# Kernel tuning notes

Hardware: AMD Instinct MI355X
Metric: run time of the kernel (lower is better)

## Reference

```python
import jax, jax.numpy as jnp
import numpy as np

C = 512
CR = C // 8  # reduced channels for b/c projections


def setup_inputs() -> dict:
    key = jax.random.key(0)
    ks = jax.random.split(key, 7)
    scale = 1.0 / np.sqrt(C)
    x = jax.random.normal(ks[0], (4, C, 64, 64), dtype=jnp.float32)
    Wb = jax.random.normal(ks[1], (CR, C), dtype=jnp.float32) * scale
    bb = jax.random.normal(ks[2], (CR,), dtype=jnp.float32) * 0.01
    Wc = jax.random.normal(ks[3], (CR, C), dtype=jnp.float32) * scale
    bc = jax.random.normal(ks[4], (CR,), dtype=jnp.float32) * 0.01
    Wd = jax.random.normal(ks[5], (C, C), dtype=jnp.float32) * scale
    bd = jax.random.normal(ks[6], (C,), dtype=jnp.float32) * 0.01
    return {"x": x, "Wb": Wb, "bb": bb, "Wc": Wc, "bc": bc, "Wd": Wd, "bd": bd}


def reference(x, Wb, bb, Wc, bc, Wd, bd):
    B, Cc, H, W = x.shape
    N = H * W
    xf = x.reshape(B, Cc, N)  # [B, C, N] (1x1 conv == per-position matmul)
    b = jnp.einsum('kc,bcn->bkn', Wb, xf) + bb[None, :, None]  # [B, CR, N]
    c = jnp.einsum('kc,bcn->bkn', Wc, xf) + bc[None, :, None]  # [B, CR, N]
    d = jnp.einsum('kc,bcn->bkn', Wd, xf) + bd[None, :, None]  # [B, C, N]
    # s[b,i,j] = sum_k b[b,k,i] * c[b,k,j]; softmax over j
    s = jnp.einsum('bki,bkj->bij', b, c)  # [B, N, N]
    s = jax.nn.softmax(s, axis=-1)
    # torch.bmm(d, s): y[b,c,j] = sum_i d[b,c,i] * s[b,i,j]
    y = jnp.einsum('bci,bij->bcj', d, s)  # [B, C, N]
    return x + y.reshape(B, Cc, H, W)
```

## Files before the change

### kernel.cpp

```cpp
#include <hip/hip_runtime.h>
#include <hip/hip_bf16.h>

typedef float f32x4 __attribute__((ext_vector_type(4)));
typedef float f32x16 __attribute__((ext_vector_type(16)));
typedef short s16x8 __attribute__((ext_vector_type(8)));
typedef uint  u32x4 __attribute__((ext_vector_type(4)));

#define MFMA_BF16(a, b, c) __builtin_amdgcn_mfma_f32_16x16x32_bf16((a), (b), (c), 0, 0, 0)
#define MFMA32(a, b, c)    __builtin_amdgcn_mfma_f32_32x32x16_bf16((a), (b), (c), 0, 0, 0)

__device__ __forceinline__ ushort f2bf(float f) {
  uint u = __builtin_bit_cast(uint, f);
  u += 0x7FFFu + ((u >> 16) & 1u);
  return (ushort)(u >> 16);
}
__device__ __forceinline__ uint pack2bf(float a, float b) {
  return (uint)f2bf(a) | ((uint)f2bf(b) << 16);
}
__device__ __forceinline__ float pexp(float s) {
  float t = fmaf(s, 1.4426950408889634f, -43.2808512266689f);
  float r;
  asm("v_exp_f32 %0, %1" : "=v"(r) : "v"(t));
  return r;
}
__device__ __forceinline__ uint cvtpk(float lo, float hi) {
  uint r;
  asm("v_cvt_pk_bf16_f32 %0, %1, %2" : "=v"(r) : "v"(lo), "v"(hi));
  return r;
}
__device__ __forceinline__ void plswap(uint& a, uint& b) {
  asm("v_permlane32_swap_b32 %0, %1" : "+v"(a), "+v"(b));
}
__device__ __forceinline__ void gld16(const void* g, void* l) {
  __builtin_amdgcn_global_load_lds(
      (const __attribute__((address_space(1))) unsigned int*)g,
      (__attribute__((address_space(3))) unsigned int*)l, 16, 0, 0);
}

#define WS_XT    0UL
#define WS_D     16777216UL
#define WS_BT    33554432UL
#define WS_CT    35651584UL
#define WS_WCAT  37748736UL
#define WS_BCAT  38404096UL

__global__ void k_prep_w(const float* __restrict__ Wb, const float* __restrict__ bb,
                         const float* __restrict__ Wc, const float* __restrict__ bc,
                         const float* __restrict__ Wd, const float* __restrict__ bd,
                         ushort* __restrict__ Wcat, float* __restrict__ bcat) {
  int idx = blockIdx.x * 256 + threadIdx.x;
  if (idx < 640 * 512) {
    int m = idx >> 9, k = idx & 511;
    float v = (m < 64) ? Wb[m * 512 + k] : (m < 128) ? Wc[(m - 64) * 512 + k] : Wd[(m - 128) * 512 + k];
    Wcat[idx] = f2bf(v);
  }
  if (idx < 640) {
    bcat[idx] = (idx < 64) ? bb[idx] : (idx < 128) ? bc[idx - 64] : bd[idx - 128];
  }
}

__global__ __launch_bounds__(256) void k_prep_xt(const float* __restrict__ x, ushort* __restrict__ xT) {
  __shared__ float tile[64][65];
  int bx = blockIdx.x;
  int b = bx >> 9;
  int c0 = ((bx >> 6) & 7) * 64;
  int n0 = (bx & 63) * 64;
  int t = threadIdx.x;
  const float* xb = x + (size_t)b * 512 * 4096;
#pragma unroll
  for (int p = 0; p < 4; ++p) {
    int cl = (t >> 4) + 16 * p;
    int nf = (t & 15) * 4;
    float4 v = *reinterpret_cast<const float4*>(xb + (size_t)(c0 + cl) * 4096 + n0 + nf);
    tile[cl][nf + 0] = v.x; tile[cl][nf + 1] = v.y; tile[cl][nf + 2] = v.z; tile[cl][nf + 3] = v.w;
  }
  __syncthreads();
  ushort* dst = xT + (size_t)b * 4096 * 512;
#pragma unroll
  for (int q = 0; q < 2; ++q) {
    int ch = t + 256 * q;
    int nl = ch >> 3;
    int cf = (ch & 7) * 8;
    uint4 o;
    o.x = pack2bf(tile[cf + 0][nl], tile[cf + 1][nl]);
    o.y = pack2bf(tile[cf + 2][nl], tile[cf + 3][nl]);
    o.z = pack2bf(tile[cf + 4][nl], tile[cf + 5][nl]);
    o.w = pack2bf(tile[cf + 6][nl], tile[cf + 7][nl]);
    *reinterpret_cast<uint4*>(dst + (size_t)(n0 + nl) * 512 + c0 + cf) = o;
  }
}

__global__ __launch_bounds__(256) void k_proj(const ushort* __restrict__ Wcat, const float* __restrict__ bcat,
                                              const ushort* __restrict__ xT, ushort* __restrict__ bT,
                                              ushort* __restrict__ cT, ushort* __restrict__ dmat) {
  int bx = blockIdx.x;
  int b = bx / 160;
  int r = bx % 160;
  int m0 = (r >> 5) * 128;
  int n0 = (r & 31) * 128;
  int t = threadIdx.x, l = t & 63, w = t >> 6;
  int wm = w >> 1, wn = w & 1, g = l >> 4, l15 = l & 15;
  const ushort* xb = xT + (size_t)b * 4096 * 512;
  f32x4 acc[4][4] = {};
  s16x8 bfn[4];
#pragma unroll
  for (int nt = 0; nt < 4; ++nt)
    bfn[nt] = *reinterpret_cast<const s16x8*>(xb + (size_t)(n0 + 64 * wn + 16 * nt + l15) * 512 + 8 * g);
  for (int k0 = 0; k0 < 512; k0 += 32) {
    s16x8 a[4], bf[4];
#pragma unroll
    for (int nt = 0; nt < 4; ++nt) bf[nt] = bfn[nt];
#pragma unroll
    for (int mt = 0; mt < 4; ++mt)
      a[mt] = *reinterpret_cast<const s16x8*>(Wcat + (size_t)(m0 + 64 * wm + 16 * mt + l15) * 512 + k0 + 8 * g);
    if (k0 + 32 < 512) {
#pragma unroll
      for (int nt = 0; nt < 4; ++nt)
        bfn[nt] = *reinterpret_cast<const s16x8*>(xb + (size_t)(n0 + 64 * wn + 16 * nt + l15) * 512 + k0 + 32 + 8 * g);
    }
    __builtin_amdgcn_sched_barrier(0);
#pragma unroll
    for (int mt = 0; mt < 4; ++mt)
#pragma unroll
      for (int nt = 0; nt < 4; ++nt)
        acc[mt][nt] = MFMA_BF16(a[mt], bf[nt], acc[mt][nt]);
  }
#pragma unroll
  for (int mt = 0; mt < 4; ++mt) {
    int mbase = m0 + 64 * wm + 16 * mt + 4 * g;
#pragma unroll
    for (int nt = 0; nt < 4; ++nt) {
      int n = n0 + 64 * wn + 16 * nt + l15;
      float vv[4];
      vv[0] = acc[mt][nt][0] + bcat[mbase + 0];
      vv[1] = acc[mt][nt][1] + bcat[mbase + 1];
      vv[2] = acc[mt][nt][2] + bcat[mbase + 2];
      vv[3] = acc[mt][nt][3] + bcat[mbase + 3];
      if (mbase < 64) {
        uint2 u2; u2.x = pack2bf(vv[0], vv[1]); u2.y = pack2bf(vv[2], vv[3]);
        size_t off = ((size_t)b * 4096 + n) * 64 + (size_t)((((mbase >> 3) ^ (n & 7)) << 3) + (mbase & 4));
        *reinterpret_cast<uint2*>(bT + off) = u2;
      } else if (mbase < 128) {
        uint2 u2; u2.x = pack2bf(vv[0], vv[1]); u2.y = pack2bf(vv[2], vv[3]);
        *reinterpret_cast<uint2*>(cT + ((size_t)b * 4096 + n) * 64 + (mbase - 64)) = u2;
      } else {
        int cc = mbase - 128;
        size_t fb = (((size_t)b * 256 + (n >> 4)) * 16) * 512;
#pragma unroll
        for (int rr = 0; rr < 4; ++rr) {
          int c = cc + rr;
          size_t idx = fb + (size_t)(c >> 5) * 512 + (size_t)(((n >> 3) & 1) * 32 + (c & 31)) * 8 + (n & 7);
          dmat[idx] = f2bf(vv[rr]);
        }
      }
    }
  }
}

__global__ __launch_bounds__(512) void k_stats(const ushort* __restrict__ bT, const ushort* __restrict__ cT,
                                               ushort* __restrict__ dmat) {
  __shared__ ushort sCT[3][8192];
  __shared__ float lsum[64];
  int bx = blockIdx.x;
  int b = bx >> 6;
  int i0 = (bx & 63) * 64;
  int t = threadIdx.x, l = t & 63, w = t >> 6;
  int wm = w >> 1, wn = w & 1, g = l >> 4, l15 = l & 15;
  if (t < 64) lsum[t] = 0.f;
  const ushort* bTb = bT + (size_t)b * 262144;
  const ushort* cTb = cT + (size_t)b * 262144;
  int arow = i0 + 16 * wm + l15;
  int r7 = arow & 7;
  const ushort* abase = bTb + (size_t)arow * 64;
  s16x8 a0 = *reinterpret_cast<const s16x8*>(abase + ((g ^ r7) << 3));
  s16x8 a1 = *reinterpret_cast<const s16x8*>(abase + (((g + 4) ^ r7) << 3));

  auto STAGE = [&](int jt) {
#pragma unroll
    for (int q = 0; q < 2; ++q) {
      int idx = t + 512 * q;
      int row = idx >> 3, u = idx & 7;
      gld16(cTb + (size_t)(jt * 128 + row) * 64 + ((u ^ (row & 7)) << 3),
            &sCT[jt % 3][idx * 8]);
    }
  };
  STAGE(0); STAGE(1);
  asm volatile("s_waitcnt vmcnt(2)" ::: "memory");
  __syncthreads();

  float lacc[4] = {0.f, 0.f, 0.f, 0.f};
  for (int jt = 0; jt < 32; ++jt) {
    if (jt + 2 < 32) STAGE(jt + 2);
    __builtin_amdgcn_sched_barrier(0);
    const ushort* cbuf = &sCT[jt % 3][0];
#pragma unroll
    for (int nt = 0; nt < 4; ++nt) {
      int row = 64 * wn + 16 * nt + l15;
      int rs = row & 7;
      s16x8 b0 = *reinterpret_cast<const s16x8*>(cbuf + row * 64 + ((g ^ rs) << 3));
      s16x8 b1 = *reinterpret_cast<const s16x8*>(cbuf + row * 64 + (((g + 4) ^ rs) << 3));
      f32x4 s = {0.f, 0.f, 0.f, 0.f};
      s = MFMA_BF16(a0, b0, s);
      s = MFMA_BF16(a1, b1, s);
#pragma unroll
      for (int rr = 0; rr < 4; ++rr) lacc[rr] += pexp(s[rr]);
    }
    if (jt < 30) { asm volatile("s_waitcnt vmcnt(2)" ::: "memory"); }
    else         { asm volatile("s_waitcnt vmcnt(0)" ::: "memory"); }
    __builtin_amdgcn_s_barrier();
  }
#pragma unroll
  for (int off = 1; off < 16; off <<= 1)
#pragma unroll
    for (int rr = 0; rr < 4; ++rr) lacc[rr] += __shfl_xor(lacc[rr], off);
  if (l15 == 0) {
#pragma unroll
    for (int rr = 0; rr < 4; ++rr) atomicAdd(&lsum[16 * wm + 4 * g + rr], lacc[rr]);
  }
  __syncthreads();
  if (t < 64) lsum[t] = 1.0f / fmaxf(lsum[t], 1e-30f);
  __syncthreads();
  int c = t;
  size_t rowb = (size_t)(c >> 5) * 512 + (size_t)(c & 31) * 8;
#pragma unroll
  for (int q = 0; q < 8; ++q) {
    int ic = (i0 >> 4) + (q >> 1);
    size_t idx = (((size_t)b * 256 + ic) * 16) * 512 + rowb + (size_t)(q & 1) * 256;
    s16x8 v = *reinterpret_cast<s16x8*>(dmat + idx);
    s16x8 nv;
#pragma unroll
    for (int e = 0; e < 8; ++e) {
      float f = __builtin_bit_cast(float, ((uint)(ushort)v[e]) << 16) * lsum[q * 8 + e];
      nv[e] = (short)f2bf(f);
    }
    *reinterpret_cast<s16x8*>(dmat + idx) = nv;
  }
}

__global__ __launch_bounds__(512, 2) void k_attn(const ushort* __restrict__ bT, const ushort* __restrict__ cT,
                                                 const ushort* __restrict__ dmat,
                                                 const float* __restrict__ x, float* __restrict__ out) {
  __shared__ ushort sBT[3][4096];
  __shared__ ushort sP[2][8192];
  int bid = blockIdx.x;
  int gid = (bid & 7) * 64 + (bid >> 3);
  int b   = gid >> 7;
  int cb  = (gid >> 5) & 3;
  int jB  = gid & 31;
  int t = threadIdx.x, w = t >> 6, l = t & 63;
  int l31 = l & 31, hi = l >> 5;
  int it_s = w >> 2, jt_s = w & 3;
  int cg = w >> 1, jg = w & 1;
  const ushort* bTb = bT + (size_t)b * 262144;
  const ushort* cTb = cT + (size_t)b * 262144;

  int js = jB * 128 + jt_s * 32 + l31;
  s16x8 cf[4];
#pragma unroll
  for (int kc = 0; kc < 4; ++kc)
    cf[kc] = *reinterpret_cast<const s16x8*>(cTb + (size_t)js * 64 + kc * 16 + hi * 8);

  int ctg = cb * 4 + cg;
  f32x16 zero16;
#pragma unroll
  for (int r = 0; r < 16; ++r) zero16[r] = 0.f;
  f32x16 yacc[2];
  yacc[0] = zero16; yacc[1] = zero16;

  auto STAGE = [&](int it) {
    gld16(bTb + (size_t)it * 4096 + (size_t)t * 8, &sBT[it % 3][t * 8]);
  };

  STAGE(0); STAGE(1);
  asm volatile("s_waitcnt vmcnt(1)" ::: "memory");
  __builtin_amdgcn_s_barrier();
  __builtin_amdgcn_sched_barrier(0);

  for (int it = 0; it < 64; ++it) {
    s16x8 dv[4];
#pragma unroll
    for (int ch = 0; ch < 4; ++ch)
      dv[ch] = *reinterpret_cast<const s16x8*>(
          dmat + ((((size_t)b * 256 + (4 * it + ch)) * 16 + ctg) * 64 + l) * 8);
    if (it + 2 < 64) STAGE(it + 2);
    __builtin_amdgcn_sched_barrier(0);
    const ushort* bbuf = &sBT[it % 3][0];
    f32x16 sv = zero16;
    __builtin_amdgcn_s_setprio(1);
#pragma unroll
    for (int kc = 0; kc < 4; ++kc) {
      const s16x8 bfv = *reinterpret_cast<const s16x8*>(
          bbuf + (32 * it_s + l31) * 64 + (((2 * kc + hi) ^ (l31 & 7)) << 3));
      sv = MFMA32(bfv, cf[kc], sv);
    }
    __builtin_amdgcn_s_setprio(0);
    float p[16];
#pragma unroll
    for (int r = 0; r < 16; ++r) p[r] = pexp(sv[r]);
    uint x0 = cvtpk(p[0], p[1]),   y0 = cvtpk(p[4], p[5]);
    uint x1 = cvtpk(p[2], p[3]),   y1 = cvtpk(p[6], p[7]);
    uint x2 = cvtpk(p[8], p[9]),   y2 = cvtpk(p[12], p[13]);
    uint x3 = cvtpk(p[10], p[11]), y3 = cvtpk(p[14], p[15]);
    plswap(x0, y0); plswap(x1, y1); plswap(x2, y2); plswap(x3, y3);
    u32x4 pw0 = {x0, x1, y0, y1};
    u32x4 pw1 = {x2, x3, y2, y3};
    ushort* pbuf = &sP[it & 1][0];
    int fi0 = jt_s * 4 + 2 * it_s;
    *reinterpret_cast<s16x8*>(pbuf + (fi0 * 64 + l) * 8)       = __builtin_bit_cast(s16x8, pw0);
    *reinterpret_cast<s16x8*>(pbuf + ((fi0 + 1) * 64 + l) * 8) = __builtin_bit_cast(s16x8, pw1);
    asm volatile("s_waitcnt lgkmcnt(0)" ::: "memory");
    __builtin_amdgcn_s_barrier();
    if (it < 62) { asm volatile("s_waitcnt vmcnt(1)" ::: "memory"); }
    else         { asm volatile("s_waitcnt vmcnt(0)" ::: "memory"); }
    __builtin_amdgcn_sched_barrier(0);
    __builtin_amdgcn_s_setprio(1);
#pragma unroll
    for (int ch = 0; ch < 4; ++ch) {
#pragma unroll
      for (int jj = 0; jj < 2; ++jj) {
        int jt = 2 * jg + jj;
        const s16x8 pfv = *reinterpret_cast<const s16x8*>(pbuf + ((jt * 4 + ch) * 64 + l) * 8);
        yacc[jj] = MFMA32(dv[ch], pfv, yacc[jj]);
      }
    }
    __builtin_amdgcn_s_setprio(0);
  }

#pragma unroll
  for (int jj = 0; jj < 2; ++jj) {
#pragma unroll
    for (int r = 0; r < 16; ++r) {
      int row = cb * 128 + cg * 32 + (r & 3) + 8 * (r >> 2) + 4 * hi;
      int col = jB * 128 + (2 * jg + jj) * 32 + l31;
      size_t idx = ((size_t)b * 512 + row) * 4096 + col;
      out[idx] = x[idx] + yacc[jj][r];
    }
  }
}

extern "C" void kernel_launch(void* const* d_in, const int* in_sizes, int n_in,
                              void* d_out, int out_size, void* d_ws, size_t ws_size,
                              hipStream_t stream) {
  const float* x  = (const float*)d_in[0];
  const float* Wb = (const float*)d_in[1];
  const float* bb = (const float*)d_in[2];
  const float* Wc = (const float*)d_in[3];
  const float* bc = (const float*)d_in[4];
  const float* Wd = (const float*)d_in[5];
  const float* bd = (const float*)d_in[6];
  char* ws = (char*)d_ws;
  ushort* xT   = (ushort*)(ws + WS_XT);
  ushort* dmat = (ushort*)(ws + WS_D);
  ushort* bT   = (ushort*)(ws + WS_BT);
  ushort* cT   = (ushort*)(ws + WS_CT);
  ushort* Wcat = (ushort*)(ws + WS_WCAT);
  float*  bcat = (float*)(ws + WS_BCAT);
  float*  out  = (float*)d_out;

  k_prep_w<<<1280, 256, 0, stream>>>(Wb, bb, Wc, bc, Wd, bd, Wcat, bcat);
  k_prep_xt<<<2048, 256, 0, stream>>>(x, xT);
  k_proj<<<640, 256, 0, stream>>>(Wcat, bcat, xT, bT, cT, dmat);
  k_stats<<<256, 512, 0, stream>>>(bT, cT, dmat);
  k_attn<<<512, 512, 0, stream>>>(bT, cT, dmat, x, out);
}
```

Before: 207.5 us.

## Materialize exponentiated attention scores once in workspace instead of recomputing per channel block

The stats kernel now computes exp(b^T c) once per row block, writes the bf16 probabilities to a large workspace buffer in MFMA fragment layout, and also accumulates row sums. The attention kernel then streams those precomputed probabilities and the normalized d tiles through shared memory and only does the d·P matmul. This removes the repeated score MFMA and exp work across the four channel blocks, at the cost of writing and re-reading a 128 MB intermediate from global memory. The old path is kept as a fallback when the workspace is too small.

```diff
diff --git a/kernel.cpp b/kernel.cpp
--- a/kernel.cpp
+++ b/kernel.cpp
@@ -43,6 +43,8 @@
 #define WS_CT    35651584UL
 #define WS_WCAT  37748736UL
 #define WS_BCAT  38404096UL
+#define WS_E     41943040UL
+#define WS_E_NEED (WS_E + 134217728UL)
 
 __global__ void k_prep_w(const float* __restrict__ Wb, const float* __restrict__ bb,
                          const float* __restrict__ Wc, const float* __restrict__ bc,
@@ -157,8 +159,181 @@
   }
 }
 
-__global__ __launch_bounds__(512) void k_stats(const ushort* __restrict__ bT, const ushort* __restrict__ cT,
-                                               ushort* __restrict__ dmat) {
+__global__ __launch_bounds__(512) void k_stats_e(const ushort* __restrict__ bT, const ushort* __restrict__ cT,
+                                                 ushort* __restrict__ dmat, ushort* __restrict__ E) {
+  __shared__ ushort sCT[3][8192];
+  __shared__ float lsum[64];
+  int bx = blockIdx.x;
+  int b = bx >> 6;
+  int IC = bx & 63;
+  int i0 = IC * 64;
+  int t = threadIdx.x, w = t >> 6, l = t & 63;
+  int l31 = l & 31, hi = l >> 5;
+  int it_s = w & 1, Jl = w >> 1;
+  if (t < 64) lsum[t] = 0.f;
+  const ushort* bTb = bT + (size_t)b * 262144;
+  const ushort* cTb = cT + (size_t)b * 262144;
+  int ri = i0 + 32 * it_s + l31;
+  int r7 = ri & 7;
+  s16x8 af[4];
+#pragma unroll
+  for (int kc = 0; kc < 4; ++kc)
+    af[kc] = *reinterpret_cast<const s16x8*>(bTb + (size_t)ri * 64 + (((2 * kc + hi) ^ r7) << 3));
+  __builtin_amdgcn_sched_barrier(0);
+  auto STAGE = [&](int st) {
+#pragma unroll
+    for (int q = 0; q < 2; ++q) {
+      int idx = t + 512 * q;
+      int row = idx >> 3, u = idx & 7;
+      gld16(cTb + (size_t)(st * 128 + row) * 64 + ((u ^ (row & 7)) << 3), &sCT[st % 3][idx * 8]);
+    }
+  };
+  STAGE(0); STAGE(1);
+  asm volatile("s_waitcnt vmcnt(2)" ::: "memory");
+  __syncthreads();
+
+  f32x16 zero16;
+#pragma unroll
+  for (int r = 0; r < 16; ++r) zero16[r] = 0.f;
+  float lacc[16];
+#pragma unroll
+  for (int r = 0; r < 16; ++r) lacc[r] = 0.f;
+
+  for (int st = 0; st < 32; ++st) {
+    if (st + 2 < 32) STAGE(st + 2);
+    __builtin_amdgcn_sched_barrier(0);
+    const ushort* cbuf = &sCT[st % 3][0];
+    int rj = Jl * 32 + l31;
+    int j7 = rj & 7;
+    f32x16 sv = zero16;
+    __builtin_amdgcn_s_setprio(1);
+#pragma unroll
+    for (int kc = 0; kc < 4; ++kc) {
+      s16x8 cfv = *reinterpret_cast<const s16x8*>(cbuf + rj * 64 + (((2 * kc + hi) ^ j7) << 3));
+      sv = MFMA32(af[kc], cfv, sv);
+    }
+    __builtin_amdgcn_s_setprio(0);
+    float p[16];
+#pragma unroll
+    for (int r = 0; r < 16; ++r) { p[r] = pexp(sv[r]); lacc[r] += p[r]; }
+    uint x0 = cvtpk(p[0], p[1]),   y0 = cvtpk(p[4], p[5]);
+    uint x1 = cvtpk(p[2], p[3]),   y1 = cvtpk(p[6], p[7]);
+    uint x2 = cvtpk(p[8], p[9]),   y2 = cvtpk(p[12], p[13]);
+    uint x3 = cvtpk(p[10], p[11]), y3 = cvtpk(p[14], p[15]);
+    plswap(x0, y0); plswap(x1, y1); plswap(x2, y2); plswap(x3, y3);
+    u32x4 pw0 = {x0, x1, y0, y1};
+    u32x4 pw1 = {x2, x3, y2, y3};
+    int J = st * 4 + Jl;
+    size_t fb = (((size_t)b * 64 + IC) * 128 + J) * 4 + 2 * it_s;
+    *reinterpret_cast<u32x4*>(E + (fb * 64 + l) * 8)       = pw0;
+    *reinterpret_cast<u32x4*>(E + ((fb + 1) * 64 + l) * 8) = pw1;
+    asm volatile("s_waitcnt vmcnt(4)" ::: "memory");
+    __builtin_amdgcn_s_barrier();
+  }
+#pragma unroll
+  for (int off = 1; off < 32; off <<= 1)
+#pragma unroll
+    for (int r = 0; r < 16; ++r) lacc[r] += __shfl_xor(lacc[r], off);
+  if (l31 == 0) {
+#pragma unroll
+    for (int r = 0; r < 16; ++r)
+      atomicAdd(&lsum[32 * it_s + (r & 3) + 8 * (r >> 2) + 4 * hi], lacc[r]);
+  }
+  __syncthreads();
+  if (t < 64) lsum[t] = 1.0f / fmaxf(lsum[t], 1e-30f);
+  __syncthreads();
+  int c = t;
+  size_t rowb = (size_t)(c >> 5) * 512 + (size_t)(c & 31) * 8;
+#pragma unroll
+  for (int q = 0; q < 8; ++q) {
+    int ic = (i0 >> 4) + (q >> 1);
+    size_t idx = (((size_t)b * 256 + ic) * 16) * 512 + rowb + (size_t)(q & 1) * 256;
+    s16x8 v = *reinterpret_cast<s16x8*>(dmat + idx);
+    s16x8 nv;
+#pragma unroll
+    for (int e = 0; e < 8; ++e) {
+      float f = __builtin_bit_cast(float, ((uint)(ushort)v[e]) << 16) * lsum[q * 8 + e];
+      nv[e] = (short)f2bf(f);
+    }
+    *reinterpret_cast<s16x8*>(dmat + idx) = nv;
+  }
+}
+
+__global__ __launch_bounds__(512, 2) void k_attn_e(const ushort* __restrict__ dmat, const ushort* __restrict__ E,
+                                                   const float* __restrict__ x, float* __restrict__ out) {
+  __shared__ ushort sE[2][8192];
+  __shared__ ushort sD[2][8192];
+  int bid = blockIdx.x;
+  int gid = (bid & 7) * 64 + (bid >> 3);
+  int b = gid >> 7, cb = (gid >> 5) & 3, jB = gid & 31;
+  int t = threadIdx.x, w = t >> 6, l = t & 63;
+  int l31 = l & 31, hi = l >> 5;
+  int cg = w >> 1, jg = w & 1;
+  f32x16 zero16;
+#pragma unroll
+  for (int r = 0; r < 16; ++r) zero16[r] = 0.f;
+  f32x16 yacc[2];
+  yacc[0] = zero16; yacc[1] = zero16;
+
+  auto STAGE = [&](int buf, int it) {
+    const ushort* ebase = E + ((((size_t)b * 64 + it) * 128 + jB * 4) * 4) * 512;
+    const ushort* dbase = dmat + (((size_t)b * 256 + 4 * it) * 16 + cb * 4) * 512;
+#pragma unroll
+    for (int q = 0; q < 2; ++q) {
+      int id = t + 512 * q;
+      gld16(ebase + (size_t)id * 8, &sE[buf][id * 8]);
+    }
+#pragma unroll
+    for (int q = 0; q < 2; ++q) {
+      int id = t + 512 * q;
+      gld16(dbase + (size_t)(id >> 8) * 8192 + (size_t)(id & 255) * 8, &sD[buf][id * 8]);
+    }
+  };
+
+  STAGE(0, 0);
+  asm volatile("s_waitcnt vmcnt(0)" ::: "memory");
+  __builtin_amdgcn_s_barrier();
+  __builtin_amdgcn_sched_barrier(0);
+
+  int buf = 0;
+  for (int it = 0; it < 64; ++it) {
+    if (it + 1 < 64) STAGE(buf ^ 1, it + 1);
+    __builtin_amdgcn_sched_barrier(0);
+    const ushort* eb = &sE[buf][0];
+    const ushort* db = &sD[buf][0];
+    s16x8 dv[4];
+#pragma unroll
+    for (int ch = 0; ch < 4; ++ch)
+      dv[ch] = *reinterpret_cast<const s16x8*>(db + ((ch * 4 + cg) * 64 + l) * 8);
+    __builtin_amdgcn_s_setprio(1);
+#pragma unroll
+    for (int ch = 0; ch < 4; ++ch) {
+#pragma unroll
+      for (int jj = 0; jj < 2; ++jj) {
+        s16x8 pfv = *reinterpret_cast<const s16x8*>(eb + (((2 * jg + jj) * 4 + ch) * 64 + l) * 8);
+        yacc[jj] = MFMA32(dv[ch], pfv, yacc[jj]);
+      }
+    }
+    __builtin_amdgcn_s_setprio(0);
+    __builtin_amdgcn_sched_barrier(0);
+    asm volatile("s_waitcnt vmcnt(0)" ::: "memory");
+    __builtin_amdgcn_s_barrier();
+    buf ^= 1;
+  }
+#pragma unroll
+  for (int jj = 0; jj < 2; ++jj) {
+#pragma unroll
+    for (int r = 0; r < 16; ++r) {
+      int row = cb * 128 + cg * 32 + (r & 3) + 8 * (r >> 2) + 4 * hi;
+      int col = jB * 128 + (2 * jg + jj) * 32 + l31;
+      size_t idx = ((size_t)b * 512 + row) * 4096 + col;
+      out[idx] = x[idx] + yacc[jj][r];
+    }
+  }
+}
+
+__global__ __launch_bounds__(512) void k_stats_f(const ushort* __restrict__ bT, const ushort* __restrict__ cT,
+                                                 ushort* __restrict__ dmat) {
   __shared__ ushort sCT[3][8192];
   __shared__ float lsum[64];
   int bx = blockIdx.x;
@@ -174,20 +349,17 @@
   const ushort* abase = bTb + (size_t)arow * 64;
   s16x8 a0 = *reinterpret_cast<const s16x8*>(abase + ((g ^ r7) << 3));
   s16x8 a1 = *reinterpret_cast<const s16x8*>(abase + (((g + 4) ^ r7) << 3));
-
   auto STAGE = [&](int jt) {
 #pragma unroll
     for (int q = 0; q < 2; ++q) {
       int idx = t + 512 * q;
       int row = idx >> 3, u = idx & 7;
-      gld16(cTb + (size_t)(jt * 128 + row) * 64 + ((u ^ (row & 7)) << 3),
-            &sCT[jt % 3][idx * 8]);
+      gld16(cTb + (size_t)(jt * 128 + row) * 64 + ((u ^ (row & 7)) << 3), &sCT[jt % 3][idx * 8]);
     }
   };
   STAGE(0); STAGE(1);
   asm volatile("s_waitcnt vmcnt(2)" ::: "memory");
   __syncthreads();
-
   float lacc[4] = {0.f, 0.f, 0.f, 0.f};
   for (int jt = 0; jt < 32; ++jt) {
     if (jt + 2 < 32) STAGE(jt + 2);
@@ -237,9 +409,9 @@
   }
 }
 
-__global__ __launch_bounds__(512, 2) void k_attn(const ushort* __restrict__ bT, const ushort* __restrict__ cT,
-                                                 const ushort* __restrict__ dmat,
-                                                 const float* __restrict__ x, float* __restrict__ out) {
+__global__ __launch_bounds__(512, 2) void k_attn_f(const ushort* __restrict__ bT, const ushort* __restrict__ cT,
+                                                   const ushort* __restrict__ dmat,
+                                                   const float* __restrict__ x, float* __restrict__ out) {
   __shared__ ushort sBT[3][4096];
   __shared__ ushort sP[2][8192];
   int bid = blockIdx.x;
@@ -253,29 +425,24 @@
   int cg = w >> 1, jg = w & 1;
   const ushort* bTb = bT + (size_t)b * 262144;
   const ushort* cTb = cT + (size_t)b * 262144;
-
   int js = jB * 128 + jt_s * 32 + l31;
   s16x8 cf[4];
 #pragma unroll
   for (int kc = 0; kc < 4; ++kc)
     cf[kc] = *reinterpret_cast<const s16x8*>(cTb + (size_t)js * 64 + kc * 16 + hi * 8);
-
   int ctg = cb * 4 + cg;
   f32x16 zero16;
 #pragma unroll
   for (int r = 0; r < 16; ++r) zero16[r] = 0.f;
   f32x16 yacc[2];
   yacc[0] = zero16; yacc[1] = zero16;
-
   auto STAGE = [&](int it) {
     gld16(bTb + (size_t)it * 4096 + (size_t)t * 8, &sBT[it % 3][t * 8]);
   };
-
   STAGE(0); STAGE(1);
   asm volatile("s_waitcnt vmcnt(1)" ::: "memory");
   __builtin_amdgcn_s_barrier();
   __builtin_amdgcn_sched_barrier(0);
-
   for (int it = 0; it < 64; ++it) {
     s16x8 dv[4];
 #pragma unroll
@@ -325,7 +492,6 @@
     }
     __builtin_amdgcn_s_setprio(0);
   }
-
 #pragma unroll
   for (int jj = 0; jj < 2; ++jj) {
 #pragma unroll
@@ -355,11 +521,17 @@
   ushort* cT   = (ushort*)(ws + WS_CT);
   ushort* Wcat = (ushort*)(ws + WS_WCAT);
   float*  bcat = (float*)(ws + WS_BCAT);
+  ushort* E    = (ushort*)(ws + WS_E);
   float*  out  = (float*)d_out;
 
   k_prep_w<<<1280, 256, 0, stream>>>(Wb, bb, Wc, bc, Wd, bd, Wcat, bcat);
   k_prep_xt<<<2048, 256, 0, stream>>>(x, xT);
   k_proj<<<640, 256, 0, stream>>>(Wcat, bcat, xT, bT, cT, dmat);
-  k_stats<<<256, 512, 0, stream>>>(bT, cT, dmat);
-  k_attn<<<512, 512, 0, stream>>>(bT, cT, dmat, x, out);
-}
+  if (ws_size >= WS_E_NEED) {
+    k_stats_e<<<256, 512, 0, stream>>>(bT, cT, dmat, E);
+    k_attn_e<<<512, 512, 0, stream>>>(dmat, E, x, out);
+  } else {
+    k_stats_f<<<256, 512, 0, stream>>>(bT, cT, dmat);
+    k_attn_f<<<512, 512, 0, stream>>>(bT, cT, dmat, x, out);
+  }
+}
```

Result: faster. 186.0 us (median of 3 runs) (-10.4%).
